# Optimization experiments

Measured on AMD Instinct MI355X. Metric: run time of the kernel, lower is better.

Reference implementation:

```python
import jax, jax.numpy as jnp
import numpy as np

EPS = 1e-6

def _rmsnorm(h, w):
    # RMSNorm: h * rsqrt(mean(h^2)) * w
    var = jnp.mean(jnp.square(h), axis=-1, keepdims=True)
    return h * jax.lax.rsqrt(var + EPS) * w

def setup_inputs() -> dict:
    key = jax.random.key(0)
    ks = jax.random.split(key, 9)
    B, N, L, D, C = 2, 4096, 256, 2048, 6
    s = 0.02
    return {
        "x": jax.random.normal(ks[0], (B, N, D), jnp.float32),
        "text_emb": jax.random.normal(ks[1], (B, L, D), jnp.float32),
        "Wc": jax.random.normal(ks[2], (C, D), jnp.float32) * s,
        "Wq": jax.random.normal(ks[3], (D, D), jnp.float32) * s,
        "Wk": jax.random.normal(ks[4], (D, D), jnp.float32) * s,
        "Wv": jax.random.normal(ks[5], (D, D), jnp.float32) * s,
        "Wo": jax.random.normal(ks[6], (D, D), jnp.float32) * s,
        "blend_weights": jnp.ones((C,), jnp.float32) / C + jax.random.normal(ks[7], (C,), jnp.float32) * 0.1,
        "surreal_gate": jnp.zeros((1,), jnp.float32),
        "norm_weight": jnp.ones((D,), jnp.float32),
        "is_surreal": 1,
    }

def reference(x, text_emb, Wc, Wq, Wk, Wv, Wo, blend_weights, surreal_gate, norm_weight, is_surreal):
    B, N, D = x.shape
    # soft concept clustering over text tokens
    cluster_logits = jnp.einsum('bld,cd->blc', text_emb, Wc)
    cluster_weights = jax.nn.softmax(cluster_logits, axis=-1)
    concept_reps = jnp.einsum('blc,bld->bcd', cluster_weights, text_emb)  # (B,C,D)
    # SDPA with a single key/value per concept: softmax over 1 key == 1, so the
    # attention output is exactly v broadcast over the N query tokens (q and k
    # cancel out of the math entirely; their grads are zero).
    v = jnp.einsum('bcd,ed->bce', concept_reps, Wv)  # (B,C,D) == per-concept output
    blend = jax.nn.softmax(blend_weights, axis=0)
    fused_bd = jnp.einsum('c,bcd->bd', blend, v)  # (B,D)
    if is_surreal:
        gate = jax.nn.sigmoid(surreal_gate)  # (1,)
        contradiction = jnp.var(v, axis=1, ddof=1)  # torch .var() is unbiased
        fused_bd = fused_bd + gate * contradiction * 0.3
    # broadcast to (B,N,D) as the torch module materializes, then norm + out_proj
    fused = jnp.broadcast_to(fused_bd[:, None, :], (B, N, D))
    out = jnp.einsum('bnd,ed->bne', _rmsnorm(fused, norm_weight), Wo)
    return x + out
```

## Files before the change

### kernel.cpp

```cpp
#include <hip/hip_runtime.h>
#include <hip/hip_bf16.h>

#define BB 2
#define NN 4096
#define LL 256
#define DD 2048
#define CC 6
#define EPSF 1e-6f

typedef float floatx4 __attribute__((ext_vector_type(4)));

__device__ __forceinline__ float dot4(float4 a, float4 b) {
    return a.x * b.x + a.y * b.y + a.z * b.z + a.w * b.w;
}

__global__ __launch_bounds__(256) void k_cluster(const float* __restrict__ te,
                                                 const float* __restrict__ Wc,
                                                 float* __restrict__ cw) {
    const int tid = threadIdx.x;
    const int row = blockIdx.x;
    const float4* t4 = (const float4*)(te + (size_t)row * DD);
    float p[CC];
#pragma unroll
    for (int c = 0; c < CC; ++c) p[c] = 0.f;
#pragma unroll
    for (int it = 0; it < 2; ++it) {
        const int i = it * 256 + tid;
        const float4 xv = t4[i];
#pragma unroll
        for (int c = 0; c < CC; ++c)
            p[c] += dot4(xv, ((const float4*)(Wc + (size_t)c * DD))[i]);
    }
#pragma unroll
    for (int c = 0; c < CC; ++c)
        for (int off = 32; off; off >>= 1) p[c] += __shfl_down(p[c], off);
    __shared__ float sred[4][CC];
    const int lane = tid & 63, wid = tid >> 6;
    if (lane == 0) {
#pragma unroll
        for (int c = 0; c < CC; ++c) sred[wid][c] = p[c];
    }
    __syncthreads();
    if (tid == 0) {
        float lg[CC], m = -1e30f;
#pragma unroll
        for (int c = 0; c < CC; ++c) {
            lg[c] = sred[0][c] + sred[1][c] + sred[2][c] + sred[3][c];
            m = fmaxf(m, lg[c]);
        }
        float s = 0.f;
#pragma unroll
        for (int c = 0; c < CC; ++c) { lg[c] = __expf(lg[c] - m); s += lg[c]; }
        const float inv = 1.f / s;
#pragma unroll
        for (int c = 0; c < CC; ++c) cw[row * CC + c] = lg[c] * inv;
    }
}

__global__ __launch_bounds__(256) void k_creps(const float* __restrict__ te,
                                               const float* __restrict__ cw,
                                               float* __restrict__ cr) {
    const int tid = threadIdx.x;
    const int b = blockIdx.x >> 6;
    const int d0 = (blockIdx.x & 63) * 32;
    const int dl = tid & 31;
    const int lc = tid >> 5;
    __shared__ float scw[LL * CC];
    __shared__ float sacc[8][32][CC];
    for (int i = tid; i < LL * CC; i += 256) scw[i] = cw[b * LL * CC + i];
    __syncthreads();
    float acc[CC];
#pragma unroll
    for (int c = 0; c < CC; ++c) acc[c] = 0.f;
    const float* tb = te + ((size_t)b * LL + lc * 32) * DD + d0 + dl;
    for (int l = 0; l < 32; ++l) {
        const float xv = tb[(size_t)l * DD];
        const int gl = lc * 32 + l;
#pragma unroll
        for (int c = 0; c < CC; ++c) acc[c] = fmaf(scw[gl * CC + c], xv, acc[c]);
    }
#pragma unroll
    for (int c = 0; c < CC; ++c) sacc[lc][dl][c] = acc[c];
    __syncthreads();
    if (tid < 32) {
#pragma unroll
        for (int c = 0; c < CC; ++c) {
            float s = 0.f;
#pragma unroll
            for (int k = 0; k < 8; ++k) s += sacc[k][tid][c];
            cr[((size_t)b * CC + c) * DD + d0 + tid] = s;
        }
    }
}

__global__ __launch_bounds__(256) void k_vfuse(const float* __restrict__ cr,
                                               const float* __restrict__ Wv,
                                               const float* __restrict__ blendw,
                                               const float* __restrict__ sgate,
                                               const int* __restrict__ issur,
                                               float* __restrict__ fused) {
    const int tid = threadIdx.x;
    const int lane = tid & 63, wid = tid >> 6;
    const int p = wid >> 1, h = wid & 1;
    const int e0 = blockIdx.x * 4 + p * 2;
    float acc[BB][2][CC];
#pragma unroll
    for (int b = 0; b < BB; ++b)
#pragma unroll
        for (int j = 0; j < 2; ++j)
#pragma unroll
            for (int c = 0; c < CC; ++c) acc[b][j][c] = 0.f;
#pragma unroll
    for (int it = 0; it < 4; ++it) {
        const int d = h * 1024 + it * 256 + lane * 4;
        const float4 w0 = *(const float4*)(Wv + (size_t)e0 * DD + d);
        const float4 w1 = *(const float4*)(Wv + (size_t)(e0 + 1) * DD + d);
#pragma unroll
        for (int b = 0; b < BB; ++b)
#pragma unroll
            for (int c = 0; c < CC; ++c) {
                const float4 cv = *(const float4*)(cr + ((size_t)b * CC + c) * DD + d);
                acc[b][0][c] += dot4(cv, w0);
                acc[b][1][c] += dot4(cv, w1);
            }
    }
#pragma unroll
    for (int b = 0; b < BB; ++b)
#pragma unroll
        for (int j = 0; j < 2; ++j)
#pragma unroll
            for (int c = 0; c < CC; ++c)
                for (int off = 32; off; off >>= 1)
                    acc[b][j][c] += __shfl_down(acc[b][j][c], off);
    __shared__ float sred[2][2][BB][2][CC];
    if (lane == 0) {
#pragma unroll
        for (int b = 0; b < BB; ++b)
#pragma unroll
            for (int j = 0; j < 2; ++j)
#pragma unroll
                for (int c = 0; c < CC; ++c) sred[p][h][b][j][c] = acc[b][j][c];
    }
    __syncthreads();
    if (h == 0 && lane == 0) {
        float bw[CC], m = -1e30f;
#pragma unroll
        for (int c = 0; c < CC; ++c) { bw[c] = blendw[c]; m = fmaxf(m, bw[c]); }
        float s = 0.f;
#pragma unroll
        for (int c = 0; c < CC; ++c) { bw[c] = __expf(bw[c] - m); s += bw[c]; }
        const float inv = 1.f / s;
#pragma unroll
        for (int c = 0; c < CC; ++c) bw[c] *= inv;
        const float gate = 1.f / (1.f + __expf(-sgate[0]));
        const int sur = issur[0];
#pragma unroll
        for (int b = 0; b < BB; ++b)
#pragma unroll
            for (int j = 0; j < 2; ++j) {
                float vv[CC];
#pragma unroll
                for (int c = 0; c < CC; ++c)
                    vv[c] = sred[p][0][b][j][c] + sred[p][1][b][j][c];
                float f = 0.f, mean = 0.f;
#pragma unroll
                for (int c = 0; c < CC; ++c) { f = fmaf(bw[c], vv[c], f); mean += vv[c]; }
                mean *= (1.f / CC);
                float var = 0.f;
#pragma unroll
                for (int c = 0; c < CC; ++c) {
                    const float dv = vv[c] - mean;
                    var = fmaf(dv, dv, var);
                }
                var *= (1.f / (CC - 1));
                if (sur) f = fmaf(gate * var, 0.3f, f);
                fused[b * DD + e0 + j] = f;
            }
    }
}

__global__ __launch_bounds__(256) void k_rmsout(const float* __restrict__ fused,
                                                const float* __restrict__ nw,
                                                const float* __restrict__ Wo,
                                                float* __restrict__ o) {
    const int tid = threadIdx.x;
    const int lane = tid & 63, wid = tid >> 6;
    float ss[BB];
#pragma unroll
    for (int b = 0; b < BB; ++b) ss[b] = 0.f;
#pragma unroll
    for (int k = 0; k < DD / 256; ++k) {
        const int d = k * 256 + tid;
#pragma unroll
        for (int b = 0; b < BB; ++b) {
            const float v = fused[b * DD + d];
            ss[b] = fmaf(v, v, ss[b]);
        }
    }
#pragma unroll
    for (int b = 0; b < BB; ++b)
        for (int off = 32; off; off >>= 1) ss[b] += __shfl_down(ss[b], off);
    __shared__ float sred0[4][BB];
    __shared__ float sscale[BB];
    if (lane == 0) {
#pragma unroll
        for (int b = 0; b < BB; ++b) sred0[wid][b] = ss[b];
    }
    __syncthreads();
    if (tid == 0) {
#pragma unroll
        for (int b = 0; b < BB; ++b) {
            const float tot = sred0[0][b] + sred0[1][b] + sred0[2][b] + sred0[3][b];
            sscale[b] = rsqrtf(tot * (1.f / DD) + EPSF);
        }
    }
    __syncthreads();
    const int p = wid >> 1, h = wid & 1;
    const int e0 = blockIdx.x * 4 + p * 2;
    float acc[BB][2];
#pragma unroll
    for (int b = 0; b < BB; ++b)
#pragma unroll
        for (int j = 0; j < 2; ++j) acc[b][j] = 0.f;
#pragma unroll
    for (int it = 0; it < 4; ++it) {
        const int d = h * 1024 + it * 256 + lane * 4;
        const float4 nv = *(const float4*)(nw + d);
        float4 w0 = *(const float4*)(Wo + (size_t)e0 * DD + d);
        float4 w1 = *(const float4*)(Wo + (size_t)(e0 + 1) * DD + d);
        w0.x *= nv.x; w0.y *= nv.y; w0.z *= nv.z; w0.w *= nv.w;
        w1.x *= nv.x; w1.y *= nv.y; w1.z *= nv.z; w1.w *= nv.w;
#pragma unroll
        for (int b = 0; b < BB; ++b) {
            const float4 fv = *(const float4*)(fused + (size_t)b * DD + d);
            acc[b][0] += dot4(fv, w0);
            acc[b][1] += dot4(fv, w1);
        }
    }
#pragma unroll
    for (int b = 0; b < BB; ++b)
#pragma unroll
        for (int j = 0; j < 2; ++j)
            for (int off = 32; off; off >>= 1) acc[b][j] += __shfl_down(acc[b][j], off);
    __shared__ float sred1[2][2][BB][2];
    if (lane == 0) {
#pragma unroll
        for (int b = 0; b < BB; ++b)
#pragma unroll
            for (int j = 0; j < 2; ++j) sred1[p][h][b][j] = acc[b][j];
    }
    __syncthreads();
    if (h == 0 && lane == 0) {
#pragma unroll
        for (int b = 0; b < BB; ++b)
#pragma unroll
            for (int j = 0; j < 2; ++j)
                o[b * DD + e0 + j] = (sred1[p][0][b][j] + sred1[p][1][b][j]) * sscale[b];
    }
}

__global__ __launch_bounds__(256) void k_add(const float* __restrict__ x,
                                             const float* __restrict__ o,
                                             float* __restrict__ out) {
    const size_t total4 = (size_t)BB * NN * DD / 4;
    const floatx4* x4 = (const floatx4*)x;
    const floatx4* o4 = (const floatx4*)o;
    floatx4* out4 = (floatx4*)out;
    for (size_t f = (size_t)blockIdx.x * 256 + threadIdx.x; f < total4;
         f += (size_t)2048 * 256) {
        const int e4 = (int)(f & (DD / 4 - 1));
        const int b = (int)(f >> 21);
        const floatx4 xv = x4[f];
        const floatx4 ov = o4[b * (DD / 4) + e4];
        const floatx4 r = xv + ov;
        __builtin_nontemporal_store(r, &out4[f]);
    }
}

extern "C" void kernel_launch(void* const* d_in, const int* in_sizes, int n_in,
                              void* d_out, int out_size, void* d_ws, size_t ws_size,
                              hipStream_t stream) {
    const float* x  = (const float*)d_in[0];
    const float* te = (const float*)d_in[1];
    const float* Wc = (const float*)d_in[2];
    const float* Wv = (const float*)d_in[5];
    const float* Wo = (const float*)d_in[6];
    const float* bw = (const float*)d_in[7];
    const float* sg = (const float*)d_in[8];
    const float* nw = (const float*)d_in[9];
    const int* isur = (const int*)d_in[10];
    float* out = (float*)d_out;

    float* ws     = (float*)d_ws;
    float* cw     = ws;
    float* cr     = ws + 4096;
    float* fusedv = ws + 4096 + 24576;
    float* o      = fusedv + 4096;

    hipLaunchKernelGGL(k_cluster, dim3(BB * LL), dim3(256), 0, stream, te, Wc, cw);
    hipLaunchKernelGGL(k_creps,   dim3(BB * 64), dim3(256), 0, stream, te, cw, cr);
    hipLaunchKernelGGL(k_vfuse,   dim3(DD / 4), dim3(256), 0, stream,
                       cr, Wv, bw, sg, isur, fusedv);
    hipLaunchKernelGGL(k_rmsout,  dim3(DD / 4), dim3(256), 0, stream,
                       fusedv, nw, Wo, o);
    hipLaunchKernelGGL(k_add,     dim3(2048), dim3(256), 0, stream, x, o, out);
}
```

Before: 50.71 us.

## Fuse four front-end kernels into one persistent kernel with grid barriers

Merges the cluster, concept-rep, V-projection/blend and RMSNorm/out-projection kernels into one 512-block kernel separated by atomic-counter grid barriers, with a memset to reset the counters each call. This removes three kernel launch gaps and their tail effects on the small front-end stages. In exchange it relies on all 512 blocks being co-resident (regular launch, not cooperative), which can deadlock if occupancy is insufficient. It also adds spin-wait barrier latency and idles most blocks during the 128-block stage.

```diff
diff --git a/kernel.cpp b/kernel.cpp
--- a/kernel.cpp
+++ b/kernel.cpp
@@ -7,6 +7,7 @@
 #define DD 2048
 #define CC 6
 #define EPSF 1e-6f
+#define FGRID 512
 
 typedef float floatx4 __attribute__((ext_vector_type(4)));
 
@@ -14,248 +15,256 @@
     return a.x * b.x + a.y * b.y + a.z * b.z + a.w * b.w;
 }
 
-__global__ __launch_bounds__(256) void k_cluster(const float* __restrict__ te,
-                                                 const float* __restrict__ Wc,
-                                                 float* __restrict__ cw) {
-    const int tid = threadIdx.x;
-    const int row = blockIdx.x;
-    const float4* t4 = (const float4*)(te + (size_t)row * DD);
-    float p[CC];
-#pragma unroll
-    for (int c = 0; c < CC; ++c) p[c] = 0.f;
-#pragma unroll
-    for (int it = 0; it < 2; ++it) {
-        const int i = it * 256 + tid;
-        const float4 xv = t4[i];
+__device__ __forceinline__ void gbar(int* cnt, int nb) {
+    __syncthreads();
+    if (threadIdx.x == 0) {
+        __threadfence();
+        __hip_atomic_fetch_add(cnt, 1, __ATOMIC_ACQ_REL, __HIP_MEMORY_SCOPE_AGENT);
+        while (__hip_atomic_load(cnt, __ATOMIC_RELAXED, __HIP_MEMORY_SCOPE_AGENT) < nb)
+            __builtin_amdgcn_s_sleep(8);
+        __threadfence();
+    }
+    __syncthreads();
+}
+
+__global__ __launch_bounds__(256, 4) void k_front(
+    const float* __restrict__ te, const float* __restrict__ Wc,
+    const float* __restrict__ Wv, const float* __restrict__ Wo,
+    const float* __restrict__ blendw, const float* __restrict__ sgate,
+    const int* __restrict__ issur, const float* __restrict__ nw,
+    float* __restrict__ cw, float* __restrict__ cr,
+    float* __restrict__ fused, float* __restrict__ o,
+    int* __restrict__ bars)
+{
+    __shared__ float smem[3072];
+    __shared__ float sredC[2][2][BB][2][CC];
+    __shared__ float sredD0[4][BB];
+    __shared__ float sscale[BB];
+    __shared__ float sredD1[2][2][BB][2];
+    const int bid = blockIdx.x, tid = threadIdx.x;
+    const int lane = tid & 63, wid = tid >> 6;
+
+    {
+        const float4* t4 = (const float4*)(te + (size_t)bid * DD);
+        float p[CC];
+#pragma unroll
+        for (int c = 0; c < CC; ++c) p[c] = 0.f;
+#pragma unroll
+        for (int it = 0; it < 2; ++it) {
+            const int i = it * 256 + tid;
+            const float4 xv = t4[i];
+#pragma unroll
+            for (int c = 0; c < CC; ++c)
+                p[c] += dot4(xv, ((const float4*)(Wc + (size_t)c * DD))[i]);
+        }
 #pragma unroll
         for (int c = 0; c < CC; ++c)
-            p[c] += dot4(xv, ((const float4*)(Wc + (size_t)c * DD))[i]);
-    }
-#pragma unroll
-    for (int c = 0; c < CC; ++c)
-        for (int off = 32; off; off >>= 1) p[c] += __shfl_down(p[c], off);
-    __shared__ float sred[4][CC];
-    const int lane = tid & 63, wid = tid >> 6;
-    if (lane == 0) {
-#pragma unroll
-        for (int c = 0; c < CC; ++c) sred[wid][c] = p[c];
-    }
-    __syncthreads();
-    if (tid == 0) {
-        float lg[CC], m = -1e30f;
-#pragma unroll
-        for (int c = 0; c < CC; ++c) {
-            lg[c] = sred[0][c] + sred[1][c] + sred[2][c] + sred[3][c];
-            m = fmaxf(m, lg[c]);
-        }
-        float s = 0.f;
-#pragma unroll
-        for (int c = 0; c < CC; ++c) { lg[c] = __expf(lg[c] - m); s += lg[c]; }
-        const float inv = 1.f / s;
-#pragma unroll
-        for (int c = 0; c < CC; ++c) cw[row * CC + c] = lg[c] * inv;
-    }
-}
-
-__global__ __launch_bounds__(256) void k_creps(const float* __restrict__ te,
-                                               const float* __restrict__ cw,
-                                               float* __restrict__ cr) {
-    const int tid = threadIdx.x;
-    const int b = blockIdx.x >> 6;
-    const int d0 = (blockIdx.x & 63) * 32;
-    const int dl = tid & 31;
-    const int lc = tid >> 5;
-    __shared__ float scw[LL * CC];
-    __shared__ float sacc[8][32][CC];
-    for (int i = tid; i < LL * CC; i += 256) scw[i] = cw[b * LL * CC + i];
-    __syncthreads();
-    float acc[CC];
-#pragma unroll
-    for (int c = 0; c < CC; ++c) acc[c] = 0.f;
-    const float* tb = te + ((size_t)b * LL + lc * 32) * DD + d0 + dl;
-    for (int l = 0; l < 32; ++l) {
-        const float xv = tb[(size_t)l * DD];
-        const int gl = lc * 32 + l;
-#pragma unroll
-        for (int c = 0; c < CC; ++c) acc[c] = fmaf(scw[gl * CC + c], xv, acc[c]);
-    }
-#pragma unroll
-    for (int c = 0; c < CC; ++c) sacc[lc][dl][c] = acc[c];
-    __syncthreads();
-    if (tid < 32) {
-#pragma unroll
-        for (int c = 0; c < CC; ++c) {
+            for (int off = 32; off; off >>= 1) p[c] += __shfl_down(p[c], off);
+        if (lane == 0) {
+#pragma unroll
+            for (int c = 0; c < CC; ++c) smem[wid * CC + c] = p[c];
+        }
+        __syncthreads();
+        if (tid == 0) {
+            float lg[CC], m = -1e30f;
+#pragma unroll
+            for (int c = 0; c < CC; ++c) {
+                lg[c] = smem[c] + smem[CC + c] + smem[2 * CC + c] + smem[3 * CC + c];
+                m = fmaxf(m, lg[c]);
+            }
             float s = 0.f;
 #pragma unroll
-            for (int k = 0; k < 8; ++k) s += sacc[k][tid][c];
-            cr[((size_t)b * CC + c) * DD + d0 + tid] = s;
-        }
-    }
-}
-
-__global__ __launch_bounds__(256) void k_vfuse(const float* __restrict__ cr,
-                                               const float* __restrict__ Wv,
-                                               const float* __restrict__ blendw,
-                                               const float* __restrict__ sgate,
-                                               const int* __restrict__ issur,
-                                               float* __restrict__ fused) {
-    const int tid = threadIdx.x;
-    const int lane = tid & 63, wid = tid >> 6;
-    const int p = wid >> 1, h = wid & 1;
-    const int e0 = blockIdx.x * 4 + p * 2;
-    float acc[BB][2][CC];
-#pragma unroll
-    for (int b = 0; b < BB; ++b)
-#pragma unroll
-        for (int j = 0; j < 2; ++j)
-#pragma unroll
-            for (int c = 0; c < CC; ++c) acc[b][j][c] = 0.f;
-#pragma unroll
-    for (int it = 0; it < 4; ++it) {
-        const int d = h * 1024 + it * 256 + lane * 4;
-        const float4 w0 = *(const float4*)(Wv + (size_t)e0 * DD + d);
-        const float4 w1 = *(const float4*)(Wv + (size_t)(e0 + 1) * DD + d);
-#pragma unroll
-        for (int b = 0; b < BB; ++b)
+            for (int c = 0; c < CC; ++c) { lg[c] = __expf(lg[c] - m); s += lg[c]; }
+            const float inv = 1.f / s;
+#pragma unroll
+            for (int c = 0; c < CC; ++c) cw[bid * CC + c] = lg[c] * inv;
+        }
+    }
+    gbar(bars + 0, FGRID);
+
+    if (bid < 128) {
+        const int b = bid >> 6;
+        const int d0 = (bid & 63) * 32;
+        const int dl = tid & 31;
+        const int lc = tid >> 5;
+        float* scw  = smem;
+        float* sacc = smem + 1536;
+        for (int i = tid; i < LL * CC; i += 256) scw[i] = cw[b * LL * CC + i];
+        __syncthreads();
+        float acc[CC];
+#pragma unroll
+        for (int c = 0; c < CC; ++c) acc[c] = 0.f;
+        const float* tb = te + ((size_t)b * LL + lc * 32) * DD + d0 + dl;
+        for (int l = 0; l < 32; ++l) {
+            const float xv = tb[(size_t)l * DD];
+            const int gl = lc * 32 + l;
+#pragma unroll
+            for (int c = 0; c < CC; ++c) acc[c] = fmaf(scw[gl * CC + c], xv, acc[c]);
+        }
+#pragma unroll
+        for (int c = 0; c < CC; ++c) sacc[(lc * 32 + dl) * CC + c] = acc[c];
+        __syncthreads();
+        if (tid < 32) {
 #pragma unroll
             for (int c = 0; c < CC; ++c) {
-                const float4 cv = *(const float4*)(cr + ((size_t)b * CC + c) * DD + d);
-                acc[b][0][c] += dot4(cv, w0);
-                acc[b][1][c] += dot4(cv, w1);
-            }
-    }
-#pragma unroll
-    for (int b = 0; b < BB; ++b)
-#pragma unroll
-        for (int j = 0; j < 2; ++j)
-#pragma unroll
-            for (int c = 0; c < CC; ++c)
-                for (int off = 32; off; off >>= 1)
-                    acc[b][j][c] += __shfl_down(acc[b][j][c], off);
-    __shared__ float sred[2][2][BB][2][CC];
-    if (lane == 0) {
+                float s = 0.f;
+#pragma unroll
+                for (int k = 0; k < 8; ++k) s += sacc[(k * 32 + tid) * CC + c];
+                cr[((size_t)b * CC + c) * DD + d0 + tid] = s;
+            }
+        }
+    }
+    gbar(bars + 1, FGRID);
+
+    {
+        const int p = wid >> 1, h = wid & 1;
+        const int e0 = bid * 4 + p * 2;
+        float acc[BB][2][CC];
 #pragma unroll
         for (int b = 0; b < BB; ++b)
 #pragma unroll
             for (int j = 0; j < 2; ++j)
 #pragma unroll
-                for (int c = 0; c < CC; ++c) sred[p][h][b][j][c] = acc[b][j][c];
-    }
-    __syncthreads();
-    if (h == 0 && lane == 0) {
-        float bw[CC], m = -1e30f;
-#pragma unroll
-        for (int c = 0; c < CC; ++c) { bw[c] = blendw[c]; m = fmaxf(m, bw[c]); }
-        float s = 0.f;
-#pragma unroll
-        for (int c = 0; c < CC; ++c) { bw[c] = __expf(bw[c] - m); s += bw[c]; }
-        const float inv = 1.f / s;
-#pragma unroll
-        for (int c = 0; c < CC; ++c) bw[c] *= inv;
-        const float gate = 1.f / (1.f + __expf(-sgate[0]));
-        const int sur = issur[0];
-#pragma unroll
-        for (int b = 0; b < BB; ++b)
-#pragma unroll
-            for (int j = 0; j < 2; ++j) {
-                float vv[CC];
+                for (int c = 0; c < CC; ++c) acc[b][j][c] = 0.f;
+#pragma unroll
+        for (int it = 0; it < 4; ++it) {
+            const int d = h * 1024 + it * 256 + lane * 4;
+            const float4 w0 = *(const float4*)(Wv + (size_t)e0 * DD + d);
+            const float4 w1 = *(const float4*)(Wv + (size_t)(e0 + 1) * DD + d);
+#pragma unroll
+            for (int b = 0; b < BB; ++b)
+#pragma unroll
+                for (int c = 0; c < CC; ++c) {
+                    const float4 cv = *(const float4*)(cr + ((size_t)b * CC + c) * DD + d);
+                    acc[b][0][c] += dot4(cv, w0);
+                    acc[b][1][c] += dot4(cv, w1);
+                }
+        }
+#pragma unroll
+        for (int b = 0; b < BB; ++b)
+#pragma unroll
+            for (int j = 0; j < 2; ++j)
 #pragma unroll
                 for (int c = 0; c < CC; ++c)
-                    vv[c] = sred[p][0][b][j][c] + sred[p][1][b][j][c];
-                float f = 0.f, mean = 0.f;
-#pragma unroll
-                for (int c = 0; c < CC; ++c) { f = fmaf(bw[c], vv[c], f); mean += vv[c]; }
-                mean *= (1.f / CC);
-                float var = 0.f;
-#pragma unroll
-                for (int c = 0; c < CC; ++c) {
-                    const float dv = vv[c] - mean;
-                    var = fmaf(dv, dv, var);
+                    for (int off = 32; off; off >>= 1)
+                        acc[b][j][c] += __shfl_down(acc[b][j][c], off);
+        if (lane == 0) {
+#pragma unroll
+            for (int b = 0; b < BB; ++b)
+#pragma unroll
+                for (int j = 0; j < 2; ++j)
+#pragma unroll
+                    for (int c = 0; c < CC; ++c) sredC[p][h][b][j][c] = acc[b][j][c];
+        }
+        __syncthreads();
+        if ((wid & 1) == 0 && lane == 0) {
+            float bw[CC], m = -1e30f;
+#pragma unroll
+            for (int c = 0; c < CC; ++c) { bw[c] = blendw[c]; m = fmaxf(m, bw[c]); }
+            float s = 0.f;
+#pragma unroll
+            for (int c = 0; c < CC; ++c) { bw[c] = __expf(bw[c] - m); s += bw[c]; }
+            const float inv = 1.f / s;
+#pragma unroll
+            for (int c = 0; c < CC; ++c) bw[c] *= inv;
+            const float gate = 1.f / (1.f + __expf(-sgate[0]));
+            const int sur = issur[0];
+#pragma unroll
+            for (int b = 0; b < BB; ++b)
+#pragma unroll
+                for (int j = 0; j < 2; ++j) {
+                    float vv[CC];
+#pragma unroll
+                    for (int c = 0; c < CC; ++c)
+                        vv[c] = sredC[p][0][b][j][c] + sredC[p][1][b][j][c];
+                    float f = 0.f, mean = 0.f;
+#pragma unroll
+                    for (int c = 0; c < CC; ++c) { f = fmaf(bw[c], vv[c], f); mean += vv[c]; }
+                    mean *= (1.f / CC);
+                    float var = 0.f;
+#pragma unroll
+                    for (int c = 0; c < CC; ++c) {
+                        const float dv = vv[c] - mean;
+                        var = fmaf(dv, dv, var);
+                    }
+                    var *= (1.f / (CC - 1));
+                    if (sur) f = fmaf(gate * var, 0.3f, f);
+                    fused[b * DD + e0 + j] = f;
                 }
-                var *= (1.f / (CC - 1));
-                if (sur) f = fmaf(gate * var, 0.3f, f);
-                fused[b * DD + e0 + j] = f;
-            }
-    }
-}
-
-__global__ __launch_bounds__(256) void k_rmsout(const float* __restrict__ fused,
-                                                const float* __restrict__ nw,
-                                                const float* __restrict__ Wo,
-                                                float* __restrict__ o) {
-    const int tid = threadIdx.x;
-    const int lane = tid & 63, wid = tid >> 6;
-    float ss[BB];
-#pragma unroll
-    for (int b = 0; b < BB; ++b) ss[b] = 0.f;
-#pragma unroll
-    for (int k = 0; k < DD / 256; ++k) {
-        const int d = k * 256 + tid;
-#pragma unroll
-        for (int b = 0; b < BB; ++b) {
-            const float v = fused[b * DD + d];
-            ss[b] = fmaf(v, v, ss[b]);
-        }
-    }
-#pragma unroll
-    for (int b = 0; b < BB; ++b)
-        for (int off = 32; off; off >>= 1) ss[b] += __shfl_down(ss[b], off);
-    __shared__ float sred0[4][BB];
-    __shared__ float sscale[BB];
-    if (lane == 0) {
-#pragma unroll
-        for (int b = 0; b < BB; ++b) sred0[wid][b] = ss[b];
-    }
-    __syncthreads();
-    if (tid == 0) {
-#pragma unroll
-        for (int b = 0; b < BB; ++b) {
-            const float tot = sred0[0][b] + sred0[1][b] + sred0[2][b] + sred0[3][b];
-            sscale[b] = rsqrtf(tot * (1.f / DD) + EPSF);
-        }
-    }
-    __syncthreads();
-    const int p = wid >> 1, h = wid & 1;
-    const int e0 = blockIdx.x * 4 + p * 2;
-    float acc[BB][2];
-#pragma unroll
-    for (int b = 0; b < BB; ++b)
-#pragma unroll
-        for (int j = 0; j < 2; ++j) acc[b][j] = 0.f;
-#pragma unroll
-    for (int it = 0; it < 4; ++it) {
-        const int d = h * 1024 + it * 256 + lane * 4;
-        const float4 nv = *(const float4*)(nw + d);
-        float4 w0 = *(const float4*)(Wo + (size_t)e0 * DD + d);
-        float4 w1 = *(const float4*)(Wo + (size_t)(e0 + 1) * DD + d);
-        w0.x *= nv.x; w0.y *= nv.y; w0.z *= nv.z; w0.w *= nv.w;
-        w1.x *= nv.x; w1.y *= nv.y; w1.z *= nv.z; w1.w *= nv.w;
-#pragma unroll
-        for (int b = 0; b < BB; ++b) {
-            const float4 fv = *(const float4*)(fused + (size_t)b * DD + d);
-            acc[b][0] += dot4(fv, w0);
-            acc[b][1] += dot4(fv, w1);
-        }
-    }
-#pragma unroll
-    for (int b = 0; b < BB; ++b)
-#pragma unroll
-        for (int j = 0; j < 2; ++j)
-            for (int off = 32; off; off >>= 1) acc[b][j] += __shfl_down(acc[b][j], off);
-    __shared__ float sred1[2][2][BB][2];
-    if (lane == 0) {
-#pragma unroll
-        for (int b = 0; b < BB; ++b)
-#pragma unroll
-            for (int j = 0; j < 2; ++j) sred1[p][h][b][j] = acc[b][j];
-    }
-    __syncthreads();
-    if (h == 0 && lane == 0) {
+        }
+    }
+    gbar(bars + 2, FGRID);
+
+    {
+        float ss[BB];
+#pragma unroll
+        for (int b = 0; b < BB; ++b) ss[b] = 0.f;
+#pragma unroll
+        for (int k = 0; k < DD / 256; ++k) {
+            const int d = k * 256 + tid;
+#pragma unroll
+            for (int b = 0; b < BB; ++b) {
+                const float v = fused[b * DD + d];
+                ss[b] = fmaf(v, v, ss[b]);
+            }
+        }
+#pragma unroll
+        for (int b = 0; b < BB; ++b)
+            for (int off = 32; off; off >>= 1) ss[b] += __shfl_down(ss[b], off);
+        if (lane == 0) {
+#pragma unroll
+            for (int b = 0; b < BB; ++b) sredD0[wid][b] = ss[b];
+        }
+        __syncthreads();
+        if (tid == 0) {
+#pragma unroll
+            for (int b = 0; b < BB; ++b) {
+                const float tot = sredD0[0][b] + sredD0[1][b] + sredD0[2][b] + sredD0[3][b];
+                sscale[b] = rsqrtf(tot * (1.f / DD) + EPSF);
+            }
+        }
+        __syncthreads();
+        const int p = wid >> 1, h = wid & 1;
+        const int e0 = bid * 4 + p * 2;
+        float acc[BB][2];
+#pragma unroll
+        for (int b = 0; b < BB; ++b)
+#pragma unroll
+            for (int j = 0; j < 2; ++j) acc[b][j] = 0.f;
+#pragma unroll
+        for (int it = 0; it < 4; ++it) {
+            const int d = h * 1024 + it * 256 + lane * 4;
+            const float4 nv = *(const float4*)(nw + d);
+            float4 w0 = *(const float4*)(Wo + (size_t)e0 * DD + d);
+            float4 w1 = *(const float4*)(Wo + (size_t)(e0 + 1) * DD + d);
+            w0.x *= nv.x; w0.y *= nv.y; w0.z *= nv.z; w0.w *= nv.w;
+            w1.x *= nv.x; w1.y *= nv.y; w1.z *= nv.z; w1.w *= nv.w;
+#pragma unroll
+            for (int b = 0; b < BB; ++b) {
+                const float4 fv = *(const float4*)(fused + (size_t)b * DD + d);
+                acc[b][0] += dot4(fv, w0);
+                acc[b][1] += dot4(fv, w1);
+            }
+        }
 #pragma unroll
         for (int b = 0; b < BB; ++b)
 #pragma unroll
             for (int j = 0; j < 2; ++j)
-                o[b * DD + e0 + j] = (sred1[p][0][b][j] + sred1[p][1][b][j]) * sscale[b];
+                for (int off = 32; off; off >>= 1) acc[b][j] += __shfl_down(acc[b][j], off);
+        if (lane == 0) {
+#pragma unroll
+            for (int b = 0; b < BB; ++b)
+#pragma unroll
+                for (int j = 0; j < 2; ++j) sredD1[p][h][b][j] = acc[b][j];
+        }
+        __syncthreads();
+        if ((wid & 1) == 0 && lane == 0) {
+#pragma unroll
+            for (int b = 0; b < BB; ++b)
+#pragma unroll
+                for (int j = 0; j < 2; ++j)
+                    o[b * DD + e0 + j] = (sredD1[p][0][b][j] + sredD1[p][1][b][j]) * sscale[b];
+        }
     }
 }
 
@@ -296,12 +305,15 @@
     float* cr     = ws + 4096;
     float* fusedv = ws + 4096 + 24576;
     float* o      = fusedv + 4096;
-
-    hipLaunchKernelGGL(k_cluster, dim3(BB * LL), dim3(256), 0, stream, te, Wc, cw);
-    hipLaunchKernelGGL(k_creps,   dim3(BB * 64), dim3(256), 0, stream, te, cw, cr);
-    hipLaunchKernelGGL(k_vfuse,   dim3(DD / 4), dim3(256), 0, stream,
-                       cr, Wv, bw, sg, isur, fusedv);
-    hipLaunchKernelGGL(k_rmsout,  dim3(DD / 4), dim3(256), 0, stream,
-                       fusedv, nw, Wo, o);
-    hipLaunchKernelGGL(k_add,     dim3(2048), dim3(256), 0, stream, x, o, out);
-}
+    int*   bars   = (int*)(o + 4096);
+
+    hipMemsetAsync(bars, 0, 3 * sizeof(int), stream);
+    void* args[] = { (void*)&te, (void*)&Wc, (void*)&Wv, (void*)&Wo,
+                     (void*)&bw, (void*)&sg, (void*)&isur, (void*)&nw,
+                     (void*)&cw, (void*)&cr, (void*)&fusedv, (void*)&o,
+                     (void*)&bars };
+    hipLaunchKernelGGL(k_front, dim3(FGRID), dim3(256), 0, stream,
+                       te, Wc, Wv, Wo, bw, sg, isur, nw, cw, cr, fusedv, o, bars);
+    (void)args;
+    hipLaunchKernelGGL(k_add, dim3(2048), dim3(256), 0, stream, x, o, out);
+}
```

Result: slower. 177.7 us (+250.5%).
